# Optimization experiments

Measured on AMD Instinct MI355X. Metric: run time of the kernel, lower is better.

Reference implementation:

```python
import jax, jax.numpy as jnp
import numpy as np

D_K = 128
NEG_BIG = 1e32  # matches torch's -1e+32 additive mask (finite in fp32)


def setup_inputs() -> dict:
    key = jax.random.key(0)
    kq, kk, kv, kqp, kkp = jax.random.split(key, 5)
    B, M, N, d_k, d_v = 8, 2048, 2048, D_K, 128
    return {
        "queries": jax.random.normal(kq, (B, M, d_k), dtype=jnp.float32),
        "keys": jax.random.normal(kk, (B, N, d_k), dtype=jnp.float32),
        "values": jax.random.normal(kv, (B, N, d_v), dtype=jnp.float32),
        "q_pres": jax.random.randint(kqp, (B, M), 0, 2, dtype=jnp.int32),
        "k_pres": jax.random.randint(kkp, (B, N), 0, 2, dtype=jnp.int32),
    }


def reference(queries, keys, values, q_pres, k_pres):
    # routing: [B, M, N] = Q K^T with multiplicative presence masking
    routing = jnp.einsum("bmd,bnd->bmn", queries, keys)
    qp = q_pres.astype(jnp.float32)  # [B, M]
    kp = k_pres.astype(jnp.float32)  # [B, N]
    routing = routing * qp[:, :, None]
    routing = routing * kp[:, None, :]
    # additive -1e32 mask for absent keys, then scaled softmax over N
    routing = routing - (1.0 - kp[:, None, :]) * NEG_BIG
    routing = jax.nn.softmax(routing / np.sqrt(D_K).astype(np.float32), axis=-1)
    return jnp.einsum("bmn,bnv->bmv", routing, values)
```

## Files before the change

kernel.cpp:

```cpp
#include <hip/hip_runtime.h>
#include <cstddef>
#include <cstdint>

#define SEQ_M 2048
#define SEQ_N 2048
#define DKV 128
#define BN 64
#define NCH 4
#define CHKEYS (SEQ_N / NCH)
#define NKT 32
#define MT2 16
#define NREC (NCH * 8 * MT2)

typedef _Float16 f16x8 __attribute__((ext_vector_type(8)));
typedef _Float16 f16x4 __attribute__((ext_vector_type(4)));
typedef float f32x4 __attribute__((ext_vector_type(4)));

#if defined(__has_builtin)
#if __has_builtin(__builtin_amdgcn_exp2f)
#define EXP2F(x) __builtin_amdgcn_exp2f(x)
#else
#define EXP2F(x) exp2f(x)
#endif
#else
#define EXP2F(x) exp2f(x)
#endif

#define SM_SCALE 0.12751745f
#define BIG_NEG 1.2751745e31f

#define KH_OFF 0
#define VH_OFF (256 * 8192)
#define P16_OFF (2 * 256 * 8192)
#define ML_BYTE_OFF ((size_t)(P16_OFF + (size_t)NREC * 16384) * 2)
#define WS_NEED (ML_BYTE_OFF + (size_t)NREC * 256 * 4)

#define AS1 __attribute__((address_space(1)))
#define AS3 __attribute__((address_space(3)))

__device__ __forceinline__ void copy16(const void* g, void* lds_base,
                                       void* lds_lane) {
#if defined(__has_builtin) && __has_builtin(__builtin_amdgcn_global_load_lds)
  __builtin_amdgcn_global_load_lds((const AS1 void*)g, (AS3 void*)lds_base, 16,
                                   0, 0);
  (void)lds_lane;
#else
  *(f16x8*)lds_lane = *(const f16x8*)g;
#endif
}

__global__ __launch_bounds__(256) void prep(const float* __restrict__ Kg,
                                            const float* __restrict__ Vg,
                                            _Float16* __restrict__ Kh,
                                            _Float16* __restrict__ Vh) {
  const int b = blockIdx.x & 7;
  const int nt = blockIdx.x >> 3;
  const int t = threadIdx.x;
  const float* Kb = Kg + ((size_t)b * SEQ_N + nt * 64) * DKV;
  const float* Vb = Vg + ((size_t)b * SEQ_N + nt * 64) * DKV;
  _Float16* Kt_ = Kh + (size_t)(b * NKT + nt) * 8192;
  _Float16* Vt_ = Vh + (size_t)(b * NKT + nt) * 8192;
#pragma unroll
  for (int i = 0; i < 4; ++i) {
    const int idx = i * 256 + t;
    const int c = idx & 15, key = idx >> 4;
    const float* src = Kb + key * DKV + c * 8;
    const float4 a0 = *(const float4*)src;
    const float4 a1 = *(const float4*)(src + 4);
    f16x8 h;
    h[0] = (_Float16)a0.x; h[1] = (_Float16)a0.y;
    h[2] = (_Float16)a0.z; h[3] = (_Float16)a0.w;
    h[4] = (_Float16)a1.x; h[5] = (_Float16)a1.y;
    h[6] = (_Float16)a1.z; h[7] = (_Float16)a1.w;
    *(f16x8*)&Kt_[c * 512 + key * 8] = h;
  }
#pragma unroll
  for (int i = 0; i < 4; ++i) {
    const int idx = i * 256 + t;
    const int vcol = idx & 127, g = idx >> 7;
    f16x8 h;
#pragma unroll
    for (int j = 0; j < 8; ++j)
      h[j] = (_Float16)Vb[(size_t)(g * 8 + j) * DKV + vcol];
    *(f16x8*)&Vt_[vcol * 64 + ((g ^ (vcol & 7)) * 8)] = h;
  }
}

__global__ __launch_bounds__(512, 4) void attn_core3(
    const _Float16* __restrict__ Kh, const _Float16* __restrict__ Vh,
    const float* __restrict__ Qg, const int* __restrict__ QPg,
    const int* __restrict__ KPg, _Float16* __restrict__ P16,
    float* __restrict__ ML) {
  __shared__ _Float16 smem[16384 + 8 * 1152];
  _Float16* const Kt = smem;
  _Float16* const Vt = smem + 8192;

  const int tid = threadIdx.x;
  const int w = tid >> 6;
  const int lane = tid & 63;
  const int q16 = lane & 15;
  const int quad = lane >> 4;
  _Float16* const Pl = smem + 16384 + w * 1152;

  const int b = blockIdx.x & 7;
  const int rest = blockIdx.x >> 3;
  const int mt = rest & 15;
  const int chk = rest >> 4;

  const int qrow = mt * 128 + w * 16 + q16;
  const float* qptr = Qg + ((size_t)b * SEQ_M + qrow) * DKV;
  const float qs = QPg[b * SEQ_M + qrow] ? 1.0f : 0.0f;
  f16x8 qf[4];
#pragma unroll
  for (int kc = 0; kc < 4; ++kc) {
    const float4 a0 = *(const float4*)(qptr + kc * 32 + quad * 8);
    const float4 a1 = *(const float4*)(qptr + kc * 32 + quad * 8 + 4);
    f16x8 h;
    h[0] = (_Float16)(a0.x * qs); h[1] = (_Float16)(a0.y * qs);
    h[2] = (_Float16)(a0.z * qs); h[3] = (_Float16)(a0.w * qs);
    h[4] = (_Float16)(a1.x * qs); h[5] = (_Float16)(a1.y * qs);
    h[6] = (_Float16)(a1.z * qs); h[7] = (_Float16)(a1.w * qs);
    qf[kc] = h;
  }

  f32x4 o[8];
#pragma unroll
  for (int vt = 0; vt < 8; ++vt) o[vt] = (f32x4){0.f, 0.f, 0.f, 0.f};
  float m_run = -3.0e38f;
  float l_run = 0.f;

  for (int ti = 0; ti < CHKEYS / BN; ++ti) {
    const int nt = chk * 8 + ti;
    __syncthreads();

    {
      const char* gsrc =
          (w < 4) ? (const char*)(Kh + (size_t)(b * NKT + nt) * 8192) + w * 4096
                  : (const char*)(Vh + (size_t)(b * NKT + nt) * 8192) +
                        (w - 4) * 4096;
      char* ldst = (w < 4) ? (char*)Kt + w * 4096 : (char*)Vt + (w - 4) * 4096;
#pragma unroll
      for (int r = 0; r < 4; ++r)
        copy16(gsrc + r * 1024 + lane * 16, ldst + r * 1024,
               ldst + r * 1024 + lane * 16);
    }
    const unsigned long long kmask =
        __ballot(KPg[(size_t)b * SEQ_N + nt * 64 + lane] != 0);
    __syncthreads();

    f32x4 st[4];
#pragma unroll
    for (int t = 0; t < 4; ++t) st[t] = (f32x4){0.f, 0.f, 0.f, 0.f};
#pragma unroll
    for (int kc = 0; kc < 4; ++kc) {
      const f16x8 qv = qf[kc];
#pragma unroll
      for (int t = 0; t < 4; ++t) {
        const f16x8 kf =
            *(const f16x8*)&Kt[((kc * 4 + quad) * 64 + t * 16 + q16) * 8];
        st[t] = __builtin_amdgcn_mfma_f32_16x16x32_f16(kf, qv, st[t], 0, 0, 0);
      }
    }

    float s2[16];
    float mx = -3.0e38f;
#pragma unroll
    for (int t = 0; t < 4; ++t)
#pragma unroll
      for (int r = 0; r < 4; ++r) {
        const int key = t * 16 + quad * 4 + r;
        const float v =
            ((kmask >> key) & 1ull) ? st[t][r] * SM_SCALE : -BIG_NEG;
        s2[t * 4 + r] = v;
        mx = fmaxf(mx, v);
      }
    mx = fmaxf(mx, __shfl_xor(mx, 16));
    mx = fmaxf(mx, __shfl_xor(mx, 32));
    const float mnew = fmaxf(m_run, mx);
    const float alpha = EXP2F(m_run - mnew);
    m_run = mnew;

    float p[16];
    float psum = 0.f;
#pragma unroll
    for (int i = 0; i < 16; ++i) {
      p[i] = EXP2F(s2[i] - mnew);
      psum += p[i];
    }
    psum += __shfl_xor(psum, 16);
    psum += __shfl_xor(psum, 32);
    l_run = l_run * alpha + psum;

    float arow[4];
#pragma unroll
    for (int r = 0; r < 4; ++r) arow[r] = __shfl(alpha, quad * 4 + r);
#pragma unroll
    for (int vt = 0; vt < 8; ++vt) {
      o[vt][0] *= arow[0]; o[vt][1] *= arow[1];
      o[vt][2] *= arow[2]; o[vt][3] *= arow[3];
    }

#pragma unroll
    for (int t = 0; t < 4; ++t) {
      f16x4 pw;
      pw[0] = (_Float16)p[t * 4 + 0];
      pw[1] = (_Float16)p[t * 4 + 1];
      pw[2] = (_Float16)p[t * 4 + 2];
      pw[3] = (_Float16)p[t * 4 + 3];
      *(f16x4*)&Pl[q16 * 72 + t * 16 + quad * 4] = pw;
    }
    const f16x8 pf0 = *(const f16x8*)&Pl[q16 * 72 + quad * 8];
    const f16x8 pf1 = *(const f16x8*)&Pl[q16 * 72 + 32 + quad * 8];
#pragma unroll
    for (int vt = 0; vt < 8; ++vt) {
      const int vcol = vt * 16 + q16;
      const f16x8 v0 =
          *(const f16x8*)&Vt[vcol * 64 + ((quad ^ (vcol & 7)) * 8)];
      o[vt] = __builtin_amdgcn_mfma_f32_16x16x32_f16(pf0, v0, o[vt], 0, 0, 0);
      const f16x8 v1 =
          *(const f16x8*)&Vt[vcol * 64 + (((quad + 4) ^ (vcol & 7)) * 8)];
      o[vt] = __builtin_amdgcn_mfma_f32_16x16x32_f16(pf1, v1, o[vt], 0, 0, 0);
    }
  }

  float linv[4];
#pragma unroll
  for (int r = 0; r < 4; ++r) linv[r] = 1.0f / __shfl(l_run, quad * 4 + r);
  const int rec = (chk * 8 + b) * MT2 + mt;
  _Float16* ob = P16 + (size_t)rec * 16384 + (size_t)(w * 16) * 128;
#pragma unroll
  for (int vt = 0; vt < 8; ++vt)
#pragma unroll
    for (int r = 0; r < 4; ++r)
      ob[(quad * 4 + r) * 128 + vt * 16 + q16] =
          (_Float16)(o[vt][r] * linv[r]);
  if (quad == 0) {
    float* ml = ML + (size_t)rec * 256;
    ml[w * 16 + q16] = m_run;
    ml[128 + w * 16 + q16] = l_run;
  }
}

__global__ __launch_bounds__(256) void attn_combine2(
    const _Float16* __restrict__ P16, const float* __restrict__ ML,
    float* __restrict__ Og) {
  const int t = threadIdx.x;
  const int b = blockIdx.x & 7;
  const int mt = blockIdx.x >> 3;
  __shared__ float msh[NCH][128];
  __shared__ float lsh[NCH][128];
#pragma unroll
  for (int i = 0; i < 2; ++i) {
    const int idx = i * 256 + t;
    const int c = idx >> 7, row = idx & 127;
    const float* ml = ML + (size_t)((c * 8 + b) * MT2 + mt) * 256;
    msh[c][row] = ml[row];
    lsh[c][row] = ml[128 + row];
  }
  __syncthreads();
  const int colh = (t & 31) * 4;
  const int rg = t >> 5;
  const _Float16* recO[NCH];
#pragma unroll
  for (int c = 0; c < NCH; ++c)
    recO[c] = P16 + (size_t)((c * 8 + b) * MT2 + mt) * 16384;
  float* outb = Og + ((size_t)b * SEQ_M + mt * 128) * DKV;
#pragma unroll
  for (int rr = 0; rr < 16; ++rr) {
    const int row = rr * 8 + rg;
    float M = -3.0e38f;
#pragma unroll
    for (int c = 0; c < NCH; ++c) M = fmaxf(M, msh[c][row]);
    float wgt[NCH];
    float lt = 0.f;
#pragma unroll
    for (int c = 0; c < NCH; ++c) {
      wgt[c] = EXP2F(msh[c][row] - M) * lsh[c][row];
      lt += wgt[c];
    }
    const float inv = 1.0f / lt;
    f32x4 acc = (f32x4){0.f, 0.f, 0.f, 0.f};
#pragma unroll
    for (int c = 0; c < NCH; ++c) {
      const f16x4 v = *(const f16x4*)(recO[c] + (size_t)row * 128 + colh);
      acc[0] += wgt[c] * (float)v[0]; acc[1] += wgt[c] * (float)v[1];
      acc[2] += wgt[c] * (float)v[2]; acc[3] += wgt[c] * (float)v[3];
    }
    f32x4 r;
    r[0] = acc[0] * inv; r[1] = acc[1] * inv;
    r[2] = acc[2] * inv; r[3] = acc[3] * inv;
    *(f32x4*)(outb + (size_t)row * DKV + colh) = r;
  }
}

__global__ __launch_bounds__(256) void attn_fallback(
    const float* __restrict__ Qg, const float* __restrict__ Kg,
    const float* __restrict__ Vg, const int* __restrict__ QPg,
    const int* __restrict__ KPg, float* __restrict__ Og) {
  __shared__ _Float16 smem[16 * 65 * 8 + 128 * 72];
  _Float16* const Kt = smem;
  _Float16* const Vt = smem + 16 * 65 * 8;
  const int tid = threadIdx.x;
  const int w = tid >> 6;
  const int lane = tid & 63;
  const int q16 = lane & 15;
  const int quad = lane >> 4;
  _Float16* const Pl = smem + w * (16 * 72);
  const int b = blockIdx.x & 7;
  const int mb = (blockIdx.x >> 3) * 64;
  const int qrow = mb + w * 16 + q16;
  const float* qptr = Qg + ((size_t)b * SEQ_M + qrow) * DKV;
  const float qs = QPg[b * SEQ_M + qrow] ? 1.0f : 0.0f;
  f16x8 qf[4];
#pragma unroll
  for (int kc = 0; kc < 4; ++kc) {
    const float4 a0 = *(const float4*)(qptr + kc * 32 + quad * 8);
    const float4 a1 = *(const float4*)(qptr + kc * 32 + quad * 8 + 4);
    f16x8 h;
    h[0] = (_Float16)(a0.x * qs); h[1] = (_Float16)(a0.y * qs);
    h[2] = (_Float16)(a0.z * qs); h[3] = (_Float16)(a0.w * qs);
    h[4] = (_Float16)(a1.x * qs); h[5] = (_Float16)(a1.y * qs);
    h[6] = (_Float16)(a1.z * qs); h[7] = (_Float16)(a1.w * qs);
    qf[kc] = h;
  }
  f32x4 o[8];
#pragma unroll
  for (int vt = 0; vt < 8; ++vt) o[vt] = (f32x4){0.f, 0.f, 0.f, 0.f};
  float m_run = -3.0e38f, l_run = 0.f;
  const int kn = tid >> 2, ks = (tid & 3) * 32;
  const int vg = tid >> 3, vk = (tid & 7) * 8;
  for (int n0 = 0; n0 < SEQ_N; n0 += BN) {
    __syncthreads();
    {
      const float* kp_ = Kg + ((size_t)b * SEQ_N + n0 + kn) * DKV + ks;
#pragma unroll
      for (int c2 = 0; c2 < 4; ++c2) {
        const float4 a0 = *(const float4*)(kp_ + c2 * 8);
        const float4 a1 = *(const float4*)(kp_ + c2 * 8 + 4);
        f16x8 h;
        h[0] = (_Float16)a0.x; h[1] = (_Float16)a0.y;
        h[2] = (_Float16)a0.z; h[3] = (_Float16)a0.w;
        h[4] = (_Float16)a1.x; h[5] = (_Float16)a1.y;
        h[6] = (_Float16)a1.z; h[7] = (_Float16)a1.w;
        *(f16x8*)&Kt[(((ks >> 3) + c2) * 65 + kn) * 8] = h;
      }
    }
    {
      const float* vp0 = Vg + ((size_t)b * SEQ_N + n0 + vk) * DKV + vg * 4;
      float4 vv[8];
#pragma unroll
      for (int j = 0; j < 8; ++j) vv[j] = *(const float4*)(vp0 + (size_t)j * DKV);
#pragma unroll
      for (int i = 0; i < 4; ++i) {
        f16x8 h;
#pragma unroll
        for (int j = 0; j < 8; ++j) h[j] = (_Float16)(((const float*)&vv[j])[i]);
        *(f16x8*)&Vt[(vg * 4 + i) * 72 + vk] = h;
      }
    }
    const unsigned long long kmask =
        __ballot(KPg[(size_t)b * SEQ_N + n0 + lane] != 0);
    __syncthreads();
    f32x4 st[4];
#pragma unroll
    for (int t = 0; t < 4; ++t) st[t] = (f32x4){0.f, 0.f, 0.f, 0.f};
#pragma unroll
    for (int kc = 0; kc < 4; ++kc) {
      const f16x8 qv = qf[kc];
#pragma unroll
      for (int t = 0; t < 4; ++t) {
        const f16x8 kf =
            *(const f16x8*)&Kt[((kc * 4 + quad) * 65 + t * 16 + q16) * 8];
        st[t] = __builtin_amdgcn_mfma_f32_16x16x32_f16(kf, qv, st[t], 0, 0, 0);
      }
    }
    float s2[16];
    float mx = -3.0e38f;
#pragma unroll
    for (int t = 0; t < 4; ++t)
#pragma unroll
      for (int r = 0; r < 4; ++r) {
        const int key = t * 16 + quad * 4 + r;
        const float v =
            ((kmask >> key) & 1ull) ? st[t][r] * SM_SCALE : -BIG_NEG;
        s2[t * 4 + r] = v;
        mx = fmaxf(mx, v);
      }
    mx = fmaxf(mx, __shfl_xor(mx, 16));
    mx = fmaxf(mx, __shfl_xor(mx, 32));
    const float mnew = fmaxf(m_run, mx);
    const float alpha = EXP2F(m_run - mnew);
    m_run = mnew;
    float p[16];
    float psum = 0.f;
#pragma unroll
    for (int i = 0; i < 16; ++i) {
      p[i] = EXP2F(s2[i] - mnew);
      psum += p[i];
    }
    psum += __shfl_xor(psum, 16);
    psum += __shfl_xor(psum, 32);
    l_run = l_run * alpha + psum;
    float arow[4];
#pragma unroll
    for (int r = 0; r < 4; ++r) arow[r] = __shfl(alpha, quad * 4 + r);
#pragma unroll
    for (int vt = 0; vt < 8; ++vt) {
      o[vt][0] *= arow[0]; o[vt][1] *= arow[1];
      o[vt][2] *= arow[2]; o[vt][3] *= arow[3];
    }
    __syncthreads();
#pragma unroll
    for (int t = 0; t < 4; ++t) {
      f16x4 pw;
      pw[0] = (_Float16)p[t * 4 + 0];
      pw[1] = (_Float16)p[t * 4 + 1];
      pw[2] = (_Float16)p[t * 4 + 2];
      pw[3] = (_Float16)p[t * 4 + 3];
      *(f16x4*)&Pl[q16 * 72 + t * 16 + quad * 4] = pw;
    }
    const f16x8 pf0 = *(const f16x8*)&Pl[q16 * 72 + quad * 8];
    const f16x8 pf1 = *(const f16x8*)&Pl[q16 * 72 + 32 + quad * 8];
#pragma unroll
    for (int vt = 0; vt < 8; ++vt) {
      const f16x8 v0 = *(const f16x8*)&Vt[(vt * 16 + q16) * 72 + quad * 8];
      o[vt] = __builtin_amdgcn_mfma_f32_16x16x32_f16(pf0, v0, o[vt], 0, 0, 0);
      const f16x8 v1 = *(const f16x8*)&Vt[(vt * 16 + q16) * 72 + 32 + quad * 8];
      o[vt] = __builtin_amdgcn_mfma_f32_16x16x32_f16(pf1, v1, o[vt], 0, 0, 0);
    }
  }
  float linv[4];
#pragma unroll
  for (int r = 0; r < 4; ++r) linv[r] = 1.0f / __shfl(l_run, quad * 4 + r);
  float* obase = Og + ((size_t)b * SEQ_M + mb + w * 16) * DKV;
#pragma unroll
  for (int vt = 0; vt < 8; ++vt)
#pragma unroll
    for (int r = 0; r < 4; ++r)
      obase[(size_t)(quad * 4 + r) * DKV + vt * 16 + q16] = o[vt][r] * linv[r];
}

extern "C" void kernel_launch(void* const* d_in, const int* in_sizes, int n_in,
                              void* d_out, int out_size, void* d_ws,
                              size_t ws_size, hipStream_t stream) {
  const float* Q = (const float*)d_in[0];
  const float* K = (const float*)d_in[1];
  const float* V = (const float*)d_in[2];
  const int* QP = (const int*)d_in[3];
  const int* KP = (const int*)d_in[4];
  float* O = (float*)d_out;
  if (ws_size >= WS_NEED) {
    _Float16* wsh = (_Float16*)d_ws;
    _Float16* Kh = wsh + KH_OFF;
    _Float16* Vh = wsh + VH_OFF;
    _Float16* P16 = wsh + P16_OFF;
    float* ML = (float*)((char*)d_ws + ML_BYTE_OFF);
    prep<<<dim3(256), dim3(256), 0, stream>>>(K, V, Kh, Vh);
    attn_core3<<<dim3(8 * MT2 * NCH), dim3(512), 0, stream>>>(
        Kh, Vh, Q, QP, KP, P16, ML);
    attn_combine2<<<dim3(8 * MT2), dim3(256), 0, stream>>>(P16, ML, O);
  } else {
    attn_fallback<<<dim3(8 * 32), dim3(256), 0, stream>>>(Q, K, V, QP, KP, O);
  }
}
```

Baseline: 114.0 us.

## Process two 16-row query tiles per wavefront to reuse K/V LDS fragments

Each wavefront of the attention core now handles 32 query rows, as two 16-row MFMA tiles, instead of 16. The block shrinks from 8 to 4 waves, so each K and V fragment read from LDS feeds two MFMAs. This cuts LDS read traffic per FLOP and doubles independent MFMA chains per wave. The cost is roughly double the accumulator and register pressure per thread, fewer waves per block, and a larger per-wave P staging buffer, which may reduce occupancy.

Measured after the change: 113.2 us. About the same (-0.7%).

```diff
diff --git a/kernel.cpp b/kernel.cpp
--- a/kernel.cpp
+++ b/kernel.cpp
@@ -86,12 +86,12 @@
   }
 }
 
-__global__ __launch_bounds__(512, 4) void attn_core3(
+__global__ __launch_bounds__(256, 2) void attn_core4(
     const _Float16* __restrict__ Kh, const _Float16* __restrict__ Vh,
     const float* __restrict__ Qg, const int* __restrict__ QPg,
     const int* __restrict__ KPg, _Float16* __restrict__ P16,
     float* __restrict__ ML) {
-  __shared__ _Float16 smem[16384 + 8 * 1152];
+  __shared__ _Float16 smem[16384 + 4 * 2304];
   _Float16* const Kt = smem;
   _Float16* const Vt = smem + 8192;
 
@@ -100,34 +100,46 @@
   const int lane = tid & 63;
   const int q16 = lane & 15;
   const int quad = lane >> 4;
-  _Float16* const Pl = smem + 16384 + w * 1152;
+  _Float16* const Pl = smem + 16384 + w * 2304;
 
   const int b = blockIdx.x & 7;
   const int rest = blockIdx.x >> 3;
   const int mt = rest & 15;
   const int chk = rest >> 4;
 
-  const int qrow = mt * 128 + w * 16 + q16;
-  const float* qptr = Qg + ((size_t)b * SEQ_M + qrow) * DKV;
-  const float qs = QPg[b * SEQ_M + qrow] ? 1.0f : 0.0f;
-  f16x8 qf[4];
+  const int qrowA = mt * 128 + w * 32 + q16;
+  const float* qptrA = Qg + ((size_t)b * SEQ_M + qrowA) * DKV;
+  const float* qptrB = qptrA + 16 * DKV;
+  const float qsA = QPg[b * SEQ_M + qrowA] ? 1.0f : 0.0f;
+  const float qsB = QPg[b * SEQ_M + qrowA + 16] ? 1.0f : 0.0f;
+  f16x8 qfA[4], qfB[4];
 #pragma unroll
   for (int kc = 0; kc < 4; ++kc) {
-    const float4 a0 = *(const float4*)(qptr + kc * 32 + quad * 8);
-    const float4 a1 = *(const float4*)(qptr + kc * 32 + quad * 8 + 4);
+    const float4 a0 = *(const float4*)(qptrA + kc * 32 + quad * 8);
+    const float4 a1 = *(const float4*)(qptrA + kc * 32 + quad * 8 + 4);
     f16x8 h;
-    h[0] = (_Float16)(a0.x * qs); h[1] = (_Float16)(a0.y * qs);
-    h[2] = (_Float16)(a0.z * qs); h[3] = (_Float16)(a0.w * qs);
-    h[4] = (_Float16)(a1.x * qs); h[5] = (_Float16)(a1.y * qs);
-    h[6] = (_Float16)(a1.z * qs); h[7] = (_Float16)(a1.w * qs);
-    qf[kc] = h;
-  }
-
-  f32x4 o[8];
-#pragma unroll
-  for (int vt = 0; vt < 8; ++vt) o[vt] = (f32x4){0.f, 0.f, 0.f, 0.f};
-  float m_run = -3.0e38f;
-  float l_run = 0.f;
+    h[0] = (_Float16)(a0.x * qsA); h[1] = (_Float16)(a0.y * qsA);
+    h[2] = (_Float16)(a0.z * qsA); h[3] = (_Float16)(a0.w * qsA);
+    h[4] = (_Float16)(a1.x * qsA); h[5] = (_Float16)(a1.y * qsA);
+    h[6] = (_Float16)(a1.z * qsA); h[7] = (_Float16)(a1.w * qsA);
+    qfA[kc] = h;
+    const float4 b0 = *(const float4*)(qptrB + kc * 32 + quad * 8);
+    const float4 b1 = *(const float4*)(qptrB + kc * 32 + quad * 8 + 4);
+    f16x8 g;
+    g[0] = (_Float16)(b0.x * qsB); g[1] = (_Float16)(b0.y * qsB);
+    g[2] = (_Float16)(b0.z * qsB); g[3] = (_Float16)(b0.w * qsB);
+    g[4] = (_Float16)(b1.x * qsB); g[5] = (_Float16)(b1.y * qsB);
+    g[6] = (_Float16)(b1.z * qsB); g[7] = (_Float16)(b1.w * qsB);
+    qfB[kc] = g;
+  }
+
+  f32x4 oA[8], oB[8];
+#pragma unroll
+  for (int vt = 0; vt < 8; ++vt) {
+    oA[vt] = (f32x4){0.f, 0.f, 0.f, 0.f};
+    oB[vt] = (f32x4){0.f, 0.f, 0.f, 0.f};
+  }
+  float mA = -3.0e38f, lA = 0.f, mB = -3.0e38f, lB = 0.f;
 
   for (int ti = 0; ti < CHKEYS / BN; ++ti) {
     const int nt = chk * 8 + ti;
@@ -135,12 +147,12 @@
 
     {
       const char* gsrc =
-          (w < 4) ? (const char*)(Kh + (size_t)(b * NKT + nt) * 8192) + w * 4096
+          (w < 2) ? (const char*)(Kh + (size_t)(b * NKT + nt) * 8192) + w * 8192
                   : (const char*)(Vh + (size_t)(b * NKT + nt) * 8192) +
-                        (w - 4) * 4096;
-      char* ldst = (w < 4) ? (char*)Kt + w * 4096 : (char*)Vt + (w - 4) * 4096;
-#pragma unroll
-      for (int r = 0; r < 4; ++r)
+                        (w - 2) * 8192;
+      char* ldst = (w < 2) ? (char*)Kt + w * 8192 : (char*)Vt + (w - 2) * 8192;
+#pragma unroll
+      for (int r = 0; r < 8; ++r)
         copy16(gsrc + r * 1024 + lane * 16, ldst + r * 1024,
                ldst + r * 1024 + lane * 16);
     }
@@ -148,96 +160,127 @@
         __ballot(KPg[(size_t)b * SEQ_N + nt * 64 + lane] != 0);
     __syncthreads();
 
-    f32x4 st[4];
-#pragma unroll
-    for (int t = 0; t < 4; ++t) st[t] = (f32x4){0.f, 0.f, 0.f, 0.f};
+    f32x4 stA[4], stB[4];
+#pragma unroll
+    for (int t = 0; t < 4; ++t) {
+      stA[t] = (f32x4){0.f, 0.f, 0.f, 0.f};
+      stB[t] = (f32x4){0.f, 0.f, 0.f, 0.f};
+    }
 #pragma unroll
     for (int kc = 0; kc < 4; ++kc) {
-      const f16x8 qv = qf[kc];
+      const f16x8 qvA = qfA[kc];
+      const f16x8 qvB = qfB[kc];
 #pragma unroll
       for (int t = 0; t < 4; ++t) {
         const f16x8 kf =
             *(const f16x8*)&Kt[((kc * 4 + quad) * 64 + t * 16 + q16) * 8];
-        st[t] = __builtin_amdgcn_mfma_f32_16x16x32_f16(kf, qv, st[t], 0, 0, 0);
-      }
-    }
-
-    float s2[16];
-    float mx = -3.0e38f;
-#pragma unroll
-    for (int t = 0; t < 4; ++t)
+        stA[t] = __builtin_amdgcn_mfma_f32_16x16x32_f16(kf, qvA, stA[t], 0, 0, 0);
+        stB[t] = __builtin_amdgcn_mfma_f32_16x16x32_f16(kf, qvB, stB[t], 0, 0, 0);
+      }
+    }
+
+    float pA[16], pB[16];
+    {
+      float mxA = -3.0e38f, mxB = -3.0e38f;
+#pragma unroll
+      for (int t = 0; t < 4; ++t)
+#pragma unroll
+        for (int r = 0; r < 4; ++r) {
+          const int key = t * 16 + quad * 4 + r;
+          const bool on = (kmask >> key) & 1ull;
+          const float vA = on ? stA[t][r] * SM_SCALE : -BIG_NEG;
+          const float vB = on ? stB[t][r] * SM_SCALE : -BIG_NEG;
+          pA[t * 4 + r] = vA; pB[t * 4 + r] = vB;
+          mxA = fmaxf(mxA, vA); mxB = fmaxf(mxB, vB);
+        }
+      mxA = fmaxf(mxA, __shfl_xor(mxA, 16));
+      mxA = fmaxf(mxA, __shfl_xor(mxA, 32));
+      mxB = fmaxf(mxB, __shfl_xor(mxB, 16));
+      mxB = fmaxf(mxB, __shfl_xor(mxB, 32));
+      const float mnA = fmaxf(mA, mxA);
+      const float mnB = fmaxf(mB, mxB);
+      const float alA = EXP2F(mA - mnA);
+      const float alB = EXP2F(mB - mnB);
+      mA = mnA; mB = mnB;
+      float psA = 0.f, psB = 0.f;
+#pragma unroll
+      for (int i = 0; i < 16; ++i) {
+        pA[i] = EXP2F(pA[i] - mnA); psA += pA[i];
+        pB[i] = EXP2F(pB[i] - mnB); psB += pB[i];
+      }
+      psA += __shfl_xor(psA, 16); psA += __shfl_xor(psA, 32);
+      psB += __shfl_xor(psB, 16); psB += __shfl_xor(psB, 32);
+      lA = lA * alA + psA;
+      lB = lB * alB + psB;
+      float arA[4], arB[4];
 #pragma unroll
       for (int r = 0; r < 4; ++r) {
-        const int key = t * 16 + quad * 4 + r;
-        const float v =
-            ((kmask >> key) & 1ull) ? st[t][r] * SM_SCALE : -BIG_NEG;
-        s2[t * 4 + r] = v;
-        mx = fmaxf(mx, v);
-      }
-    mx = fmaxf(mx, __shfl_xor(mx, 16));
-    mx = fmaxf(mx, __shfl_xor(mx, 32));
-    const float mnew = fmaxf(m_run, mx);
-    const float alpha = EXP2F(m_run - mnew);
-    m_run = mnew;
-
-    float p[16];
-    float psum = 0.f;
-#pragma unroll
-    for (int i = 0; i < 16; ++i) {
-      p[i] = EXP2F(s2[i] - mnew);
-      psum += p[i];
-    }
-    psum += __shfl_xor(psum, 16);
-    psum += __shfl_xor(psum, 32);
-    l_run = l_run * alpha + psum;
-
-    float arow[4];
-#pragma unroll
-    for (int r = 0; r < 4; ++r) arow[r] = __shfl(alpha, quad * 4 + r);
-#pragma unroll
-    for (int vt = 0; vt < 8; ++vt) {
-      o[vt][0] *= arow[0]; o[vt][1] *= arow[1];
-      o[vt][2] *= arow[2]; o[vt][3] *= arow[3];
+        arA[r] = __shfl(alA, quad * 4 + r);
+        arB[r] = __shfl(alB, quad * 4 + r);
+      }
+#pragma unroll
+      for (int vt = 0; vt < 8; ++vt) {
+        oA[vt][0] *= arA[0]; oA[vt][1] *= arA[1];
+        oA[vt][2] *= arA[2]; oA[vt][3] *= arA[3];
+        oB[vt][0] *= arB[0]; oB[vt][1] *= arB[1];
+        oB[vt][2] *= arB[2]; oB[vt][3] *= arB[3];
+      }
     }
 
 #pragma unroll
     for (int t = 0; t < 4; ++t) {
-      f16x4 pw;
-      pw[0] = (_Float16)p[t * 4 + 0];
-      pw[1] = (_Float16)p[t * 4 + 1];
-      pw[2] = (_Float16)p[t * 4 + 2];
-      pw[3] = (_Float16)p[t * 4 + 3];
-      *(f16x4*)&Pl[q16 * 72 + t * 16 + quad * 4] = pw;
-    }
-    const f16x8 pf0 = *(const f16x8*)&Pl[q16 * 72 + quad * 8];
-    const f16x8 pf1 = *(const f16x8*)&Pl[q16 * 72 + 32 + quad * 8];
+      f16x4 pwA, pwB;
+#pragma unroll
+      for (int r = 0; r < 4; ++r) {
+        pwA[r] = (_Float16)pA[t * 4 + r];
+        pwB[r] = (_Float16)pB[t * 4 + r];
+      }
+      *(f16x4*)&Pl[q16 * 72 + t * 16 + quad * 4] = pwA;
+      *(f16x4*)&Pl[(16 + q16) * 72 + t * 16 + quad * 4] = pwB;
+    }
+    const f16x8 pfA0 = *(const f16x8*)&Pl[q16 * 72 + quad * 8];
+    const f16x8 pfA1 = *(const f16x8*)&Pl[q16 * 72 + 32 + quad * 8];
+    const f16x8 pfB0 = *(const f16x8*)&Pl[(16 + q16) * 72 + quad * 8];
+    const f16x8 pfB1 = *(const f16x8*)&Pl[(16 + q16) * 72 + 32 + quad * 8];
+
 #pragma unroll
     for (int vt = 0; vt < 8; ++vt) {
       const int vcol = vt * 16 + q16;
       const f16x8 v0 =
           *(const f16x8*)&Vt[vcol * 64 + ((quad ^ (vcol & 7)) * 8)];
-      o[vt] = __builtin_amdgcn_mfma_f32_16x16x32_f16(pf0, v0, o[vt], 0, 0, 0);
       const f16x8 v1 =
           *(const f16x8*)&Vt[vcol * 64 + (((quad + 4) ^ (vcol & 7)) * 8)];
-      o[vt] = __builtin_amdgcn_mfma_f32_16x16x32_f16(pf1, v1, o[vt], 0, 0, 0);
-    }
-  }
-
-  float linv[4];
-#pragma unroll
-  for (int r = 0; r < 4; ++r) linv[r] = 1.0f / __shfl(l_run, quad * 4 + r);
+      oA[vt] = __builtin_amdgcn_mfma_f32_16x16x32_f16(pfA0, v0, oA[vt], 0, 0, 0);
+      oA[vt] = __builtin_amdgcn_mfma_f32_16x16x32_f16(pfA1, v1, oA[vt], 0, 0, 0);
+      oB[vt] = __builtin_amdgcn_mfma_f32_16x16x32_f16(pfB0, v0, oB[vt], 0, 0, 0);
+      oB[vt] = __builtin_amdgcn_mfma_f32_16x16x32_f16(pfB1, v1, oB[vt], 0, 0, 0);
+    }
+  }
+
+  float liA[4], liB[4];
+#pragma unroll
+  for (int r = 0; r < 4; ++r) {
+    liA[r] = 1.0f / __shfl(lA, quad * 4 + r);
+    liB[r] = 1.0f / __shfl(lB, quad * 4 + r);
+  }
   const int rec = (chk * 8 + b) * MT2 + mt;
-  _Float16* ob = P16 + (size_t)rec * 16384 + (size_t)(w * 16) * 128;
+  _Float16* obA = P16 + (size_t)rec * 16384 + (size_t)(w * 32) * 128;
+  _Float16* obB = obA + 16 * 128;
 #pragma unroll
   for (int vt = 0; vt < 8; ++vt)
 #pragma unroll
-    for (int r = 0; r < 4; ++r)
-      ob[(quad * 4 + r) * 128 + vt * 16 + q16] =
-          (_Float16)(o[vt][r] * linv[r]);
+    for (int r = 0; r < 4; ++r) {
+      obA[(quad * 4 + r) * 128 + vt * 16 + q16] =
+          (_Float16)(oA[vt][r] * liA[r]);
+      obB[(quad * 4 + r) * 128 + vt * 16 + q16] =
+          (_Float16)(oB[vt][r] * liB[r]);
+    }
   if (quad == 0) {
     float* ml = ML + (size_t)rec * 256;
-    ml[w * 16 + q16] = m_run;
-    ml[128 + w * 16 + q16] = l_run;
+    ml[w * 32 + q16] = mA;
+    ml[w * 32 + 16 + q16] = mB;
+    ml[128 + w * 32 + q16] = lA;
+    ml[128 + w * 32 + 16 + q16] = lB;
   }
 }
 
@@ -456,7 +499,7 @@
     _Float16* P16 = wsh + P16_OFF;
     float* ML = (float*)((char*)d_ws + ML_BYTE_OFF);
     prep<<<dim3(256), dim3(256), 0, stream>>>(K, V, Kh, Vh);
-    attn_core3<<<dim3(8 * MT2 * NCH), dim3(512), 0, stream>>>(
+    attn_core4<<<dim3(8 * MT2 * NCH), dim3(256), 0, stream>>>(
         Kh, Vh, Q, QP, KP, P16, ML);
     attn_combine2<<<dim3(8 * MT2), dim3(256), 0, stream>>>(P16, ML, O);
   } else {
```
